# Kernel optimization log

Hardware: AMD Instinct MI355X
Metric: run time of the kernel (lower is better)

## Reference

```python
import jax, jax.numpy as jnp
import numpy as np

NUM_HEADS = 16
NUM_KV_HEADS = 4
HEAD_DIM = 64
HIDDEN = 1024
BATCH, SEQ = 2, 2048
CAUSAL = False


def _rotate_half(x):
    x1, x2 = jnp.split(x, 2, axis=-1)
    return jnp.concatenate([-x2, x1], axis=-1)


def setup_inputs() -> dict:
    key = jax.random.key(0)
    k1, k2, k3 = jax.random.split(key, 3)
    hidden_states = jax.random.normal(k1, (BATCH, SEQ, HIDDEN), dtype=jnp.float32)
    # realistic rotary tables
    inv_freq = 1.0 / (10000.0 ** (np.arange(0, HEAD_DIM, 2, dtype=np.float32) / HEAD_DIM))
    t = np.arange(SEQ, dtype=np.float32)
    freqs = np.outer(t, inv_freq)                      # [S, D/2]
    emb = np.concatenate([freqs, freqs], axis=-1)      # [S, D]
    cos = jnp.asarray(np.cos(emb), dtype=jnp.float32)
    sin = jnp.asarray(np.sin(emb), dtype=jnp.float32)
    qkv_out = (NUM_HEADS + 2 * NUM_KV_HEADS) * HEAD_DIM
    w_qkv = jax.random.normal(k2, (qkv_out, HIDDEN), dtype=jnp.float32) * (HIDDEN ** -0.5)
    w_o = jax.random.normal(k3, (HIDDEN, NUM_HEADS * HEAD_DIM), dtype=jnp.float32) * ((NUM_HEADS * HEAD_DIM) ** -0.5)
    return {"hidden_states": hidden_states, "cos": cos, "sin": sin, "w_qkv": w_qkv, "w_o": w_o}


def reference(hidden_states, cos, sin, w_qkv, w_o):
    b, s, _ = hidden_states.shape
    qkv = jnp.einsum('bsh,oh->bso', hidden_states, w_qkv)
    qkv = qkv.reshape(b, s, NUM_HEADS + 2 * NUM_KV_HEADS, HEAD_DIM)
    q = qkv[:, :, :NUM_HEADS]                                    # [b,s,Hq,d]
    k = qkv[:, :, NUM_HEADS:NUM_HEADS + NUM_KV_HEADS]            # [b,s,Hkv,d]
    v = qkv[:, :, NUM_HEADS + NUM_KV_HEADS:]                     # [b,s,Hkv,d]
    # RoPE (HF style): broadcast cos/sin [s,d] over batch and heads
    c = cos[None, :, None, :]
    sn = sin[None, :, None, :]
    q = q * c + _rotate_half(q) * sn
    k = k * c + _rotate_half(k) * sn
    # GQA: repeat kv heads to match q heads
    rep = NUM_HEADS // NUM_KV_HEADS
    k = jnp.repeat(k, rep, axis=2)
    v = jnp.repeat(v, rep, axis=2)
    scale = HEAD_DIM ** -0.5
    scores = jnp.einsum('bqhd,bkhd->bhqk', q, k) * scale
    if CAUSAL:
        mask = jnp.tril(jnp.ones((s, s), dtype=bool))
        scores = jnp.where(mask[None, None], scores, jnp.finfo(scores.dtype).min)
    probs = jax.nn.softmax(scores, axis=-1)
    attn = jnp.einsum('bhqk,bkhd->bqhd', probs, v)
    attn = attn.reshape(b, s, NUM_HEADS * HEAD_DIM)
    return jnp.einsum('bso,ho->bsh', attn, w_o)
```

## Files before the change

kernel.cpp:

```cpp
#include <hip/hip_runtime.h>
#include <hip/hip_bf16.h>

typedef unsigned short u16;
typedef unsigned int u32;
typedef __attribute__((ext_vector_type(8))) short short8;
typedef __attribute__((ext_vector_type(4))) float f32x4;
typedef __attribute__((ext_vector_type(16))) float f32x16;
typedef __attribute__((ext_vector_type(4))) u32 u32x4;

__device__ __forceinline__ u16 f2b(float f) {
    __hip_bfloat16 h = __float2bfloat16(f);
    return *reinterpret_cast<u16*>(&h);
}
__device__ __forceinline__ float b2f(u16 u) {
    __hip_bfloat16 h;
    *reinterpret_cast<u16*>(&h) = u;
    return __bfloat162float(h);
}
__device__ __forceinline__ u32 cvtpk(float lo, float hi_) {
    u32 r;
    asm("v_cvt_pk_bf16_f32 %0, %1, %2" : "=v"(r) : "v"(lo), "v"(hi_));
    return r;
}
__device__ __forceinline__ float fexp2(float x) {
    float r;
    asm("v_exp_f32 %0, %1" : "=v"(r) : "v"(x));
    return r;
}
__device__ __forceinline__ void gload16(const void* g, void* l) {
    __builtin_amdgcn_global_load_lds(
        (const __attribute__((address_space(1))) unsigned int*)g,
        (__attribute__((address_space(3))) unsigned int*)l, 16, 0, 0);
}

__global__ void convert_kernel(const float* __restrict__ X, const float* __restrict__ W1,
                               const float* __restrict__ W2,
                               u16* __restrict__ Xb, u16* __restrict__ W1b, u16* __restrict__ W2b) {
    int idx = blockIdx.x * 256 + threadIdx.x;
    const float* src; u16* dst; int off;
    if (idx < 1048576)        { src = X;  dst = Xb;  off = idx; }
    else if (idx < 1441792)   { src = W1; dst = W1b; off = idx - 1048576; }
    else                      { src = W2; dst = W2b; off = idx - 1441792; }
    float4 v = reinterpret_cast<const float4*>(src)[off];
    ushort4 o;
    o.x = f2b(v.x); o.y = f2b(v.y); o.z = f2b(v.z); o.w = f2b(v.w);
    reinterpret_cast<ushort4*>(dst)[off] = o;
}

template <typename OUT>
__global__ __launch_bounds__(256, 3) void gemm_bt(const u16* __restrict__ A, const u16* __restrict__ B,
                                                  OUT* __restrict__ C, int M, int N, int K) {
    __shared__ u16 As[2][64 * 64];
    __shared__ u16 Bs[2][128 * 64];
    const int tid = threadIdx.x;
    const int lane = tid & 63, wave = tid >> 6;
    const int wm = wave >> 1, wn = wave & 1;
    const int row16 = lane & 15, kgrp = lane >> 4;
    const int bm = blockIdx.x, bn = blockIdx.y;
    const int nk = K >> 6;

    const int r0 = tid >> 3, c0s = ((tid & 7) ^ (r0 & 7)) * 8;
    const u16* aSrc = A + (size_t)(bm * 64 + r0) * K + c0s;
    const u16* bSrc = B + (size_t)(bn * 128 + r0) * K + c0s;
    u16* const ad0 = &As[0][tid * 8];
    u16* const ad1 = &As[0][(tid + 256) * 8];
    u16* const bd0 = &Bs[0][tid * 8];
    u16* const bd1 = &Bs[0][(tid + 256) * 8];
    u16* const bd2 = &Bs[0][(tid + 512) * 8];
    u16* const bd3 = &Bs[0][(tid + 768) * 8];
    const size_t aK32 = (size_t)32 * K;

    f32x4 acc[2][4];
#pragma unroll
    for (int i = 0; i < 2; ++i)
#pragma unroll
        for (int j = 0; j < 4; ++j) acc[i][j] = {0.f, 0.f, 0.f, 0.f};

    auto stage = [&](int buf) {
        int lo = buf * 4096;
        int lob = buf * 8192;
        gload16(aSrc, ad0 + lo);
        gload16(aSrc + aK32, ad1 + lo);
        gload16(bSrc, bd0 + lob);
        gload16(bSrc + aK32, bd1 + lob);
        gload16(bSrc + 2 * aK32, bd2 + lob);
        gload16(bSrc + 3 * aK32, bd3 + lob);
        aSrc += 64; bSrc += 64;
    };

    stage(0);
    __syncthreads();
    for (int kt = 0; kt < nk; ++kt) {
        int cur = kt & 1;
        if (kt + 1 < nk) stage(cur ^ 1);
        short8 af[2][2], bfr[4][2];
#pragma unroll
        for (int mf = 0; mf < 2; ++mf) {
            int r = wm * 32 + mf * 16 + row16;
#pragma unroll
            for (int kk = 0; kk < 2; ++kk)
                af[mf][kk] = *(const short8*)&As[cur][(r * 8 + ((kk * 4 + kgrp) ^ (r & 7))) * 8];
        }
#pragma unroll
        for (int nf = 0; nf < 4; ++nf) {
            int r = wn * 64 + nf * 16 + row16;
#pragma unroll
            for (int kk = 0; kk < 2; ++kk)
                bfr[nf][kk] = *(const short8*)&Bs[cur][(r * 8 + ((kk * 4 + kgrp) ^ (r & 7))) * 8];
        }
        __builtin_amdgcn_s_setprio(1);
#pragma unroll
        for (int kk = 0; kk < 2; ++kk)
#pragma unroll
            for (int mf = 0; mf < 2; ++mf)
#pragma unroll
                for (int nf = 0; nf < 4; ++nf)
                    acc[mf][nf] = __builtin_amdgcn_mfma_f32_16x16x32_bf16(af[mf][kk], bfr[nf][kk], acc[mf][nf], 0, 0, 0);
        __builtin_amdgcn_s_setprio(0);
        __syncthreads();
    }
#pragma unroll
    for (int mf = 0; mf < 2; ++mf)
#pragma unroll
        for (int r = 0; r < 4; ++r) {
            int row = bm * 64 + wm * 32 + mf * 16 + kgrp * 4 + r;
#pragma unroll
            for (int nf = 0; nf < 4; ++nf) {
                int col = bn * 128 + wn * 64 + nf * 16 + row16;
                float v = acc[mf][nf][r];
                if constexpr (sizeof(OUT) == 2) C[(size_t)row * N + col] = f2b(v);
                else                            C[(size_t)row * N + col] = v;
            }
        }
}

__global__ void rope_kernel(const u16* __restrict__ qkv, const float* __restrict__ cosb,
                            const float* __restrict__ sinb, u16* __restrict__ Qa,
                            u16* __restrict__ Ka) {
    int idx = blockIdx.x * 256 + threadIdx.x;
    if (idx < 2097152) {
        int d = idx & 31, h = (idx >> 5) & 15, m = idx >> 9;
        int s = m & 2047, b = m >> 11;
        const u16* src = qkv + (size_t)m * 1536 + h * 64 + d;
        float q1 = b2f(src[0]), q2 = b2f(src[32]);
        float c = cosb[s * 64 + d], sn = sinb[s * 64 + d];
        u16* dst = Qa + ((size_t)(b * 16 + h) * 2048 + s) * 64 + d;
        dst[0]  = f2b((q1 * c - q2 * sn) * 0.18033688f);
        dst[32] = f2b((q2 * c + q1 * sn) * 0.18033688f);
    } else {
        int t = idx - 2097152;
        int d = t & 31, kh = (t >> 5) & 3, m = t >> 7;
        int s = m & 2047, b = m >> 11;
        const u16* src = qkv + (size_t)m * 1536 + (16 + kh) * 64 + d;
        float q1 = b2f(src[0]), q2 = b2f(src[32]);
        float c = cosb[s * 64 + d], sn = sinb[s * 64 + d];
        u16* dst = Ka + ((size_t)(b * 4 + kh) * 2048 + s) * 64 + d;
        dst[0]  = f2b(q1 * c - q2 * sn);
        dst[32] = f2b(q2 * c + q1 * sn);
    }
}

__global__ __launch_bounds__(256) void vtrans_kernel(const u16* __restrict__ qkv, u16* __restrict__ Vt) {
    __shared__ u16 T[64 * 71];
    const int tid = threadIdx.x;
    const int sblk = blockIdx.x, kh = blockIdx.y, b = blockIdx.z;
    const u16* src = qkv + (size_t)(b * 2048 + sblk * 64) * 1536 + 1280 + kh * 64;
#pragma unroll
    for (int it = 0; it < 2; ++it) {
        int u = it * 256 + tid;
        int s = u >> 3, c = u & 7;
        short8 v = *(const short8*)(src + (size_t)s * 1536 + c * 8);
#pragma unroll
        for (int i = 0; i < 8; ++i)
            T[(c * 8 + i) * 71 + s] = (u16)v[i];
    }
    __syncthreads();
    u16* dst = Vt + (size_t)(b * 4 + kh) * 64 * 2048 + sblk * 64;
#pragma unroll
    for (int it = 0; it < 2; ++it) {
        int u = it * 256 + tid;
        int d = u >> 3, s0 = (u & 7) * 8;
        short8 o;
#pragma unroll
        for (int i = 0; i < 8; ++i) o[i] = (short)T[d * 71 + s0 + i];
        *(short8*)(dst + (size_t)d * 2048 + s0) = o;
    }
}

__global__ __launch_bounds__(256, 2) void attn_kernel(const u16* __restrict__ Qa,
                                                      const u16* __restrict__ Ka,
                                                      const u16* __restrict__ Vt,
                                                      u16* __restrict__ Ob) {
    __shared__ u16 Ks[2][64 * 64];
    __shared__ u16 Vs[2][64 * 64];
    const int tid = threadIdx.x, lane = tid & 63, wave = tid >> 6;
    const int q32 = lane & 31, hi = lane >> 5;
    const int qt = blockIdx.x, h = blockIdx.y, b = blockIdx.z;
    const int kh = h >> 2;
    const u16* Qp = Qa + ((size_t)(b * 16 + h) * 2048 + qt * 128 + wave * 32) * 64;

    const int r0 = tid >> 3, c0s = ((tid & 7) ^ (r0 & 7)) * 8;
    const u16* kSrc = Ka + (size_t)(b * 4 + kh) * 2048 * 64 + (size_t)r0 * 64 + c0s;
    const u16* vSrc = Vt + (size_t)(b * 4 + kh) * 64 * 2048 + (size_t)r0 * 2048 + c0s;
    u16* const kd0 = &Ks[0][tid * 8];
    u16* const kd1 = &Ks[0][(tid + 256) * 8];
    u16* const vd0 = &Vs[0][tid * 8];
    u16* const vd1 = &Vs[0][(tid + 256) * 8];

    short8 qf[4];
#pragma unroll
    for (int dt = 0; dt < 4; ++dt)
        qf[dt] = *(const short8*)(Qp + q32 * 64 + dt * 16 + hi * 8);

    f32x16 oacc[2];
#pragma unroll
    for (int i = 0; i < 2; ++i)
#pragma unroll
        for (int r = 0; r < 16; ++r) oacc[i][r] = 0.f;
    float lpx = 0.f, lpy = 0.f;

    auto stageKV = [&](int buf) {
        int lo = buf * 4096;
        gload16(kSrc,           kd0 + lo);
        gload16(kSrc + 32 * 64, kd1 + lo);
        gload16(vSrc,             vd0 + lo);
        gload16(vSrc + 32 * 2048, vd1 + lo);
        kSrc += 4096; vSrc += 64;
    };

    stageKV(0);
    __syncthreads();
    for (int kvt = 0; kvt < 32; ++kvt) {
        const int cur = kvt & 1;
        if (kvt + 1 < 32) stageKV(cur ^ 1);

        f32x16 S[2];
#pragma unroll
        for (int j = 0; j < 2; ++j)
#pragma unroll
            for (int r = 0; r < 16; ++r) S[j][r] = 0.f;
        __builtin_amdgcn_s_setprio(1);
#pragma unroll
        for (int kt2 = 0; kt2 < 2; ++kt2) {
            int krow = kt2 * 32 + q32;
#pragma unroll
            for (int dt = 0; dt < 4; ++dt) {
                short8 kf = *(const short8*)&Ks[cur][(krow * 8 + ((dt * 2 + hi) ^ (krow & 7))) * 8];
                S[kt2] = __builtin_amdgcn_mfma_f32_32x32x16_bf16(kf, qf[dt], S[kt2], 0, 0, 0);
            }
        }
        __builtin_amdgcn_s_setprio(0);

#pragma unroll
        for (int kt2 = 0; kt2 < 2; ++kt2)
#pragma unroll
            for (int r = 0; r < 16; r += 2) {
                float p0 = fexp2(S[kt2][r]);
                float p1 = fexp2(S[kt2][r + 1]);
                S[kt2][r] = p0; S[kt2][r + 1] = p1;
                lpx += p0; lpy += p1;
            }

        __builtin_amdgcn_s_setprio(1);
#pragma unroll
        for (int kc = 0; kc < 4; ++kc) {
            const int kt2 = kc >> 1, R = (kc & 1) * 8;
            u32 a0 = cvtpk(S[kt2][R + 0], S[kt2][R + 1]);
            u32 b0 = cvtpk(S[kt2][R + 4], S[kt2][R + 5]);
            asm("v_permlane32_swap_b32 %0, %1" : "+v"(a0), "+v"(b0));
            u32 a1 = cvtpk(S[kt2][R + 2], S[kt2][R + 3]);
            u32 b1 = cvtpk(S[kt2][R + 6], S[kt2][R + 7]);
            asm("v_permlane32_swap_b32 %0, %1" : "+v"(a1), "+v"(b1));
            u32x4 pw; pw[0] = a0; pw[1] = a1; pw[2] = b0; pw[3] = b1;
            short8 pf = __builtin_bit_cast(short8, pw);
#pragma unroll
            for (int dt2 = 0; dt2 < 2; ++dt2) {
                int vrow = dt2 * 32 + q32;
                short8 vf = *(const short8*)&Vs[cur][(vrow * 8 + ((kc * 2 + hi) ^ (vrow & 7))) * 8];
                oacc[dt2] = __builtin_amdgcn_mfma_f32_32x32x16_bf16(vf, pf, oacc[dt2], 0, 0, 0);
            }
        }
        __builtin_amdgcn_s_setprio(0);
        __syncthreads();
    }

    float lpart = lpx + lpy;
    float l = lpart + __shfl_xor(lpart, 32);
    float inv = 1.f / l;
    const size_t mbase = ((size_t)(b * 2048 + qt * 128 + wave * 32 + q32)) * 1024 + h * 64;
#pragma unroll
    for (int dt2 = 0; dt2 < 2; ++dt2)
#pragma unroll
        for (int rq = 0; rq < 4; ++rq) {
            ushort4 o;
            o.x = f2b(oacc[dt2][rq * 4 + 0] * inv);
            o.y = f2b(oacc[dt2][rq * 4 + 1] * inv);
            o.z = f2b(oacc[dt2][rq * 4 + 2] * inv);
            o.w = f2b(oacc[dt2][rq * 4 + 3] * inv);
            *(ushort4*)&Ob[mbase + dt2 * 32 + rq * 8 + hi * 4] = o;
        }
}

extern "C" void kernel_launch(void* const* d_in, const int* in_sizes, int n_in,
                              void* d_out, int out_size, void* d_ws, size_t ws_size,
                              hipStream_t stream) {
    const float* X    = (const float*)d_in[0];
    const float* cosb = (const float*)d_in[1];
    const float* sinb = (const float*)d_in[2];
    const float* Wqkv = (const float*)d_in[3];
    const float* Wo   = (const float*)d_in[4];
    float* out = (float*)d_out;
    char* ws = (char*)d_ws;

    u16* Xbf    = (u16*)(ws);
    u16* Wqkvbf = (u16*)(ws + 8388608);
    u16* Wobf   = (u16*)(ws + 11534336);
    u16* QKV    = (u16*)(ws + 13631488);
    u16* Qa     = (u16*)(ws + 26214400);
    u16* Ka     = (u16*)(ws + 34603008);
    u16* Vt     = (u16*)(ws + 36700160);
    u16* attnb  = Xbf;

    convert_kernel<<<6656, 256, 0, stream>>>(X, Wqkv, Wo, Xbf, Wqkvbf, Wobf);
    gemm_bt<u16><<<dim3(64, 12), 256, 0, stream>>>(Xbf, Wqkvbf, QKV, 4096, 1536, 1024);
    rope_kernel<<<10240, 256, 0, stream>>>(QKV, cosb, sinb, Qa, Ka);
    vtrans_kernel<<<dim3(32, 4, 2), 256, 0, stream>>>(QKV, Vt);
    attn_kernel<<<dim3(16, 16, 2), 256, 0, stream>>>(Qa, Ka, Vt, attnb);
    gemm_bt<float><<<dim3(64, 8), 256, 0, stream>>>(attnb, Wobf, out, 4096, 1024, 1024);
}
```

Baseline: 166.6 us.

## Fuse RoPE into QKV GEMM epilogue and register-stage KV loads in attention

Adds a specialized QKV GEMM whose epilogue applies RoPE and scaling and writes Q and K directly in head-major layout, while V goes to a compact temporary buffer. This removes the separate rope kernel and the full QKV intermediate round trip. The attention kernel also changes from direct global-to-LDS loads to register-staged loads that are prefetched two tiles ahead, with a transposed swizzled LDS layout and an explicit waitcnt/barrier. The risks are higher register pressure and scattered 2-byte epilogue stores.

```diff
diff --git a/kernel.cpp b/kernel.cpp
--- a/kernel.cpp
+++ b/kernel.cpp
@@ -47,6 +47,266 @@
     reinterpret_cast<ushort4*>(dst)[off] = o;
 }
 
+__global__ __launch_bounds__(256, 3) void gemm_qkv(const u16* __restrict__ A, const u16* __restrict__ B,
+                                                   const float* __restrict__ cosb, const float* __restrict__ sinb,
+                                                   u16* __restrict__ Qa, u16* __restrict__ Ka,
+                                                   u16* __restrict__ Vtmp) {
+    __shared__ u16 As[2][64 * 64];
+    __shared__ u16 Bs[2][128 * 64];
+    const int tid = threadIdx.x;
+    const int lane = tid & 63, wave = tid >> 6;
+    const int wm = wave >> 1, wn = wave & 1;
+    const int row16 = lane & 15, kgrp = lane >> 4;
+    const int bm = blockIdx.x, bn = blockIdx.y;
+    const int K = 1024;
+
+    const int r0 = tid >> 3, c0s = ((tid & 7) ^ (r0 & 7)) * 8;
+    const u16* aSrc = A + (size_t)(bm * 64 + r0) * K + c0s;
+    const u16* bSrc = B + (size_t)(bn * 128 + r0) * K + c0s;
+    u16* const ad0 = &As[0][tid * 8];
+    u16* const ad1 = &As[0][(tid + 256) * 8];
+    u16* const bd0 = &Bs[0][tid * 8];
+    u16* const bd1 = &Bs[0][(tid + 256) * 8];
+    u16* const bd2 = &Bs[0][(tid + 512) * 8];
+    u16* const bd3 = &Bs[0][(tid + 768) * 8];
+    const size_t aK32 = (size_t)32 * K;
+
+    f32x4 acc[2][4];
+#pragma unroll
+    for (int i = 0; i < 2; ++i)
+#pragma unroll
+        for (int j = 0; j < 4; ++j) acc[i][j] = {0.f, 0.f, 0.f, 0.f};
+
+    auto stage = [&](int buf) {
+        int lo = buf * 4096;
+        int lob = buf * 8192;
+        gload16(aSrc, ad0 + lo);
+        gload16(aSrc + aK32, ad1 + lo);
+        gload16(bSrc, bd0 + lob);
+        gload16(bSrc + aK32, bd1 + lob);
+        gload16(bSrc + 2 * aK32, bd2 + lob);
+        gload16(bSrc + 3 * aK32, bd3 + lob);
+        aSrc += 64; bSrc += 64;
+    };
+
+    stage(0);
+    __syncthreads();
+    for (int kt = 0; kt < 16; ++kt) {
+        int cur = kt & 1;
+        if (kt + 1 < 16) stage(cur ^ 1);
+        short8 af[2][2], bfr[4][2];
+#pragma unroll
+        for (int mf = 0; mf < 2; ++mf) {
+            int r = wm * 32 + mf * 16 + row16;
+#pragma unroll
+            for (int kk = 0; kk < 2; ++kk)
+                af[mf][kk] = *(const short8*)&As[cur][(r * 8 + ((kk * 4 + kgrp) ^ (r & 7))) * 8];
+        }
+#pragma unroll
+        for (int nf = 0; nf < 4; ++nf) {
+            int r = wn * 64 + nf * 16 + row16;
+#pragma unroll
+            for (int kk = 0; kk < 2; ++kk)
+                bfr[nf][kk] = *(const short8*)&Bs[cur][(r * 8 + ((kk * 4 + kgrp) ^ (r & 7))) * 8];
+        }
+        __builtin_amdgcn_s_setprio(1);
+#pragma unroll
+        for (int kk = 0; kk < 2; ++kk)
+#pragma unroll
+            for (int mf = 0; mf < 2; ++mf)
+#pragma unroll
+                for (int nf = 0; nf < 4; ++nf)
+                    acc[mf][nf] = __builtin_amdgcn_mfma_f32_16x16x32_bf16(af[mf][kk], bfr[nf][kk], acc[mf][nf], 0, 0, 0);
+        __builtin_amdgcn_s_setprio(0);
+        __syncthreads();
+    }
+
+#pragma unroll
+    for (int mf = 0; mf < 2; ++mf)
+#pragma unroll
+        for (int r = 0; r < 4; ++r) {
+            int m = bm * 64 + wm * 32 + mf * 16 + kgrp * 4 + r;
+            int s = m & 2047, bb = m >> 11;
+            float v0 = acc[mf][0][r], v1 = acc[mf][1][r], v2 = acc[mf][2][r], v3 = acc[mf][3][r];
+            if (bn < 10) {
+                float c0 = cosb[s * 64 + row16],       c1 = cosb[s * 64 + 16 + row16];
+                float n0 = sinb[s * 64 + row16],       n1 = sinb[s * 64 + 16 + row16];
+                float o0 = v0 * c0 - v2 * n0, o1 = v1 * c1 - v3 * n1;
+                float o2 = v2 * c0 + v0 * n0, o3 = v3 * c1 + v1 * n1;
+                u16* dst;
+                if (bn < 8) {
+                    int h = bn * 2 + wn;
+                    dst = Qa + ((size_t)(bb * 16 + h) * 2048 + s) * 64;
+                    o0 *= 0.18033688f; o1 *= 0.18033688f; o2 *= 0.18033688f; o3 *= 0.18033688f;
+                } else {
+                    int kh = (bn - 8) * 2 + wn;
+                    dst = Ka + ((size_t)(bb * 4 + kh) * 2048 + s) * 64;
+                }
+                dst[row16]      = f2b(o0);
+                dst[row16 + 16] = f2b(o1);
+                dst[row16 + 32] = f2b(o2);
+                dst[row16 + 48] = f2b(o3);
+            } else {
+                u16* dst = Vtmp + (size_t)m * 256 + (bn - 10) * 128 + wn * 64;
+                dst[row16]      = f2b(v0);
+                dst[row16 + 16] = f2b(v1);
+                dst[row16 + 32] = f2b(v2);
+                dst[row16 + 48] = f2b(v3);
+            }
+        }
+}
+
+__global__ __launch_bounds__(256) void vtrans_kernel(const u16* __restrict__ Vtmp, u16* __restrict__ Vt) {
+    __shared__ u16 T[64 * 71];
+    const int tid = threadIdx.x;
+    const int sblk = blockIdx.x, kh = blockIdx.y, b = blockIdx.z;
+    const u16* src = Vtmp + (size_t)(b * 2048 + sblk * 64) * 256 + kh * 64;
+#pragma unroll
+    for (int it = 0; it < 2; ++it) {
+        int u = it * 256 + tid;
+        int s = u >> 3, c = u & 7;
+        short8 v = *(const short8*)(src + (size_t)s * 256 + c * 8);
+#pragma unroll
+        for (int i = 0; i < 8; ++i)
+            T[(c * 8 + i) * 71 + s] = (u16)v[i];
+    }
+    __syncthreads();
+    u16* dst = Vt + (size_t)(b * 4 + kh) * 64 * 2048 + sblk * 64;
+#pragma unroll
+    for (int it = 0; it < 2; ++it) {
+        int u = it * 256 + tid;
+        int d = u >> 3, s0 = (u & 7) * 8;
+        short8 o;
+#pragma unroll
+        for (int i = 0; i < 8; ++i) o[i] = (short)T[d * 71 + s0 + i];
+        *(short8*)(dst + (size_t)d * 2048 + s0) = o;
+    }
+}
+
+__global__ __launch_bounds__(256, 2) void attn_kernel(const u16* __restrict__ Qa,
+                                                      const u16* __restrict__ Ka,
+                                                      const u16* __restrict__ Vt,
+                                                      u16* __restrict__ Ob) {
+    __shared__ u16 Ks[2][4096];
+    __shared__ u16 Vs[2][4096];
+    const int tid = threadIdx.x, lane = tid & 63, wave = tid >> 6;
+    const int q32 = lane & 31, hi = lane >> 5;
+    const int qt = blockIdx.x, h = blockIdx.y, b = blockIdx.z;
+    const int kh = h >> 2;
+    const u16* Qp = Qa + ((size_t)(b * 16 + h) * 2048 + qt * 128 + wave * 32) * 64;
+
+    const int lrow = tid >> 3, lc = tid & 7;
+    const u16* kSrc = Ka + (size_t)(b * 4 + kh) * 2048 * 64 + (size_t)lrow * 64 + lc * 8;
+    const u16* vSrc = Vt + (size_t)(b * 4 + kh) * 64 * 2048 + (size_t)lrow * 2048 + lc * 8;
+    const int wk = (lc * 64 + (lrow ^ lc)) * 8;
+
+    int rb[8];
+#pragma unroll
+    for (int c = 0; c < 8; ++c) rb[c] = (c * 64 + (q32 ^ c)) * 8;
+
+    short8 qf[4];
+#pragma unroll
+    for (int dt = 0; dt < 4; ++dt)
+        qf[dt] = *(const short8*)(Qp + q32 * 64 + dt * 16 + hi * 8);
+
+    f32x16 oacc[2];
+#pragma unroll
+    for (int i = 0; i < 2; ++i)
+#pragma unroll
+        for (int r = 0; r < 16; ++r) oacc[i][r] = 0.f;
+    float lpx = 0.f, lpy = 0.f;
+
+    short8 kr0, kr1, vr0, vr1;
+    auto LOAD = [&]() {
+        kr0 = *(const short8*)kSrc;
+        kr1 = *(const short8*)(kSrc + 2048);
+        vr0 = *(const short8*)vSrc;
+        vr1 = *(const short8*)(vSrc + 65536);
+        kSrc += 4096; vSrc += 64;
+    };
+    auto WRITE = [&](int buf) {
+        *(short8*)&Ks[buf][wk]       = kr0;
+        *(short8*)&Ks[buf][wk + 256] = kr1;
+        *(short8*)&Vs[buf][wk]       = vr0;
+        *(short8*)&Vs[buf][wk + 256] = vr1;
+    };
+
+    LOAD();
+    WRITE(0);
+    LOAD();
+    asm volatile("s_waitcnt lgkmcnt(0)\n\ts_barrier" ::: "memory");
+
+    for (int kvt = 0; kvt < 32; ++kvt) {
+        const int cur = kvt & 1;
+        if (kvt + 1 < 32) WRITE(cur ^ 1);
+        if (kvt + 2 < 32) LOAD();
+
+        f32x16 S[2];
+#pragma unroll
+        for (int j = 0; j < 2; ++j)
+#pragma unroll
+            for (int r = 0; r < 16; ++r) S[j][r] = 0.f;
+        __builtin_amdgcn_s_setprio(1);
+#pragma unroll
+        for (int kt2 = 0; kt2 < 2; ++kt2) {
+#pragma unroll
+            for (int dt = 0; dt < 4; ++dt) {
+                short8 kf = *(const short8*)&Ks[cur][rb[dt * 2 + hi] + kt2 * 256];
+                S[kt2] = __builtin_amdgcn_mfma_f32_32x32x16_bf16(kf, qf[dt], S[kt2], 0, 0, 0);
+            }
+        }
+        __builtin_amdgcn_s_setprio(0);
+
+#pragma unroll
+        for (int kt2 = 0; kt2 < 2; ++kt2)
+#pragma unroll
+            for (int r = 0; r < 16; r += 2) {
+                float p0 = fexp2(S[kt2][r]);
+                float p1 = fexp2(S[kt2][r + 1]);
+                S[kt2][r] = p0; S[kt2][r + 1] = p1;
+                lpx += p0; lpy += p1;
+            }
+
+        __builtin_amdgcn_s_setprio(1);
+#pragma unroll
+        for (int kc = 0; kc < 4; ++kc) {
+            const int kt2 = kc >> 1, R = (kc & 1) * 8;
+            u32 a0 = cvtpk(S[kt2][R + 0], S[kt2][R + 1]);
+            u32 b0 = cvtpk(S[kt2][R + 4], S[kt2][R + 5]);
+            asm("v_permlane32_swap_b32 %0, %1" : "+v"(a0), "+v"(b0));
+            u32 a1 = cvtpk(S[kt2][R + 2], S[kt2][R + 3]);
+            u32 b1 = cvtpk(S[kt2][R + 6], S[kt2][R + 7]);
+            asm("v_permlane32_swap_b32 %0, %1" : "+v"(a1), "+v"(b1));
+            u32x4 pw; pw[0] = a0; pw[1] = a1; pw[2] = b0; pw[3] = b1;
+            short8 pf = __builtin_bit_cast(short8, pw);
+#pragma unroll
+            for (int dt2 = 0; dt2 < 2; ++dt2) {
+                short8 vf = *(const short8*)&Vs[cur][rb[kc * 2 + hi] + dt2 * 256];
+                oacc[dt2] = __builtin_amdgcn_mfma_f32_32x32x16_bf16(vf, pf, oacc[dt2], 0, 0, 0);
+            }
+        }
+        __builtin_amdgcn_s_setprio(0);
+
+        asm volatile("s_waitcnt lgkmcnt(0)\n\ts_barrier" ::: "memory");
+    }
+
+    float lpart = lpx + lpy;
+    float l = lpart + __shfl_xor(lpart, 32);
+    float inv = 1.f / l;
+    const size_t mbase = ((size_t)(b * 2048 + qt * 128 + wave * 32 + q32)) * 1024 + h * 64;
+#pragma unroll
+    for (int dt2 = 0; dt2 < 2; ++dt2)
+#pragma unroll
+        for (int rq = 0; rq < 4; ++rq) {
+            ushort4 o;
+            o.x = f2b(oacc[dt2][rq * 4 + 0] * inv);
+            o.y = f2b(oacc[dt2][rq * 4 + 1] * inv);
+            o.z = f2b(oacc[dt2][rq * 4 + 2] * inv);
+            o.w = f2b(oacc[dt2][rq * 4 + 3] * inv);
+            *(ushort4*)&Ob[mbase + dt2 * 32 + rq * 8 + hi * 4] = o;
+        }
+}
+
 template <typename OUT>
 __global__ __launch_bounds__(256, 3) void gemm_bt(const u16* __restrict__ A, const u16* __restrict__ B,
                                                   OUT* __restrict__ C, int M, int N, int K) {
@@ -134,173 +394,6 @@
         }
 }
 
-__global__ void rope_kernel(const u16* __restrict__ qkv, const float* __restrict__ cosb,
-                            const float* __restrict__ sinb, u16* __restrict__ Qa,
-                            u16* __restrict__ Ka) {
-    int idx = blockIdx.x * 256 + threadIdx.x;
-    if (idx < 2097152) {
-        int d = idx & 31, h = (idx >> 5) & 15, m = idx >> 9;
-        int s = m & 2047, b = m >> 11;
-        const u16* src = qkv + (size_t)m * 1536 + h * 64 + d;
-        float q1 = b2f(src[0]), q2 = b2f(src[32]);
-        float c = cosb[s * 64 + d], sn = sinb[s * 64 + d];
-        u16* dst = Qa + ((size_t)(b * 16 + h) * 2048 + s) * 64 + d;
-        dst[0]  = f2b((q1 * c - q2 * sn) * 0.18033688f);
-        dst[32] = f2b((q2 * c + q1 * sn) * 0.18033688f);
-    } else {
-        int t = idx - 2097152;
-        int d = t & 31, kh = (t >> 5) & 3, m = t >> 7;
-        int s = m & 2047, b = m >> 11;
-        const u16* src = qkv + (size_t)m * 1536 + (16 + kh) * 64 + d;
-        float q1 = b2f(src[0]), q2 = b2f(src[32]);
-        float c = cosb[s * 64 + d], sn = sinb[s * 64 + d];
-        u16* dst = Ka + ((size_t)(b * 4 + kh) * 2048 + s) * 64 + d;
-        dst[0]  = f2b(q1 * c - q2 * sn);
-        dst[32] = f2b(q2 * c + q1 * sn);
-    }
-}
-
-__global__ __launch_bounds__(256) void vtrans_kernel(const u16* __restrict__ qkv, u16* __restrict__ Vt) {
-    __shared__ u16 T[64 * 71];
-    const int tid = threadIdx.x;
-    const int sblk = blockIdx.x, kh = blockIdx.y, b = blockIdx.z;
-    const u16* src = qkv + (size_t)(b * 2048 + sblk * 64) * 1536 + 1280 + kh * 64;
-#pragma unroll
-    for (int it = 0; it < 2; ++it) {
-        int u = it * 256 + tid;
-        int s = u >> 3, c = u & 7;
-        short8 v = *(const short8*)(src + (size_t)s * 1536 + c * 8);
-#pragma unroll
-        for (int i = 0; i < 8; ++i)
-            T[(c * 8 + i) * 71 + s] = (u16)v[i];
-    }
-    __syncthreads();
-    u16* dst = Vt + (size_t)(b * 4 + kh) * 64 * 2048 + sblk * 64;
-#pragma unroll
-    for (int it = 0; it < 2; ++it) {
-        int u = it * 256 + tid;
-        int d = u >> 3, s0 = (u & 7) * 8;
-        short8 o;
-#pragma unroll
-        for (int i = 0; i < 8; ++i) o[i] = (short)T[d * 71 + s0 + i];
-        *(short8*)(dst + (size_t)d * 2048 + s0) = o;
-    }
-}
-
-__global__ __launch_bounds__(256, 2) void attn_kernel(const u16* __restrict__ Qa,
-                                                      const u16* __restrict__ Ka,
-                                                      const u16* __restrict__ Vt,
-                                                      u16* __restrict__ Ob) {
-    __shared__ u16 Ks[2][64 * 64];
-    __shared__ u16 Vs[2][64 * 64];
-    const int tid = threadIdx.x, lane = tid & 63, wave = tid >> 6;
-    const int q32 = lane & 31, hi = lane >> 5;
-    const int qt = blockIdx.x, h = blockIdx.y, b = blockIdx.z;
-    const int kh = h >> 2;
-    const u16* Qp = Qa + ((size_t)(b * 16 + h) * 2048 + qt * 128 + wave * 32) * 64;
-
-    const int r0 = tid >> 3, c0s = ((tid & 7) ^ (r0 & 7)) * 8;
-    const u16* kSrc = Ka + (size_t)(b * 4 + kh) * 2048 * 64 + (size_t)r0 * 64 + c0s;
-    const u16* vSrc = Vt + (size_t)(b * 4 + kh) * 64 * 2048 + (size_t)r0 * 2048 + c0s;
-    u16* const kd0 = &Ks[0][tid * 8];
-    u16* const kd1 = &Ks[0][(tid + 256) * 8];
-    u16* const vd0 = &Vs[0][tid * 8];
-    u16* const vd1 = &Vs[0][(tid + 256) * 8];
-
-    short8 qf[4];
-#pragma unroll
-    for (int dt = 0; dt < 4; ++dt)
-        qf[dt] = *(const short8*)(Qp + q32 * 64 + dt * 16 + hi * 8);
-
-    f32x16 oacc[2];
-#pragma unroll
-    for (int i = 0; i < 2; ++i)
-#pragma unroll
-        for (int r = 0; r < 16; ++r) oacc[i][r] = 0.f;
-    float lpx = 0.f, lpy = 0.f;
-
-    auto stageKV = [&](int buf) {
-        int lo = buf * 4096;
-        gload16(kSrc,           kd0 + lo);
-        gload16(kSrc + 32 * 64, kd1 + lo);
-        gload16(vSrc,             vd0 + lo);
-        gload16(vSrc + 32 * 2048, vd1 + lo);
-        kSrc += 4096; vSrc += 64;
-    };
-
-    stageKV(0);
-    __syncthreads();
-    for (int kvt = 0; kvt < 32; ++kvt) {
-        const int cur = kvt & 1;
-        if (kvt + 1 < 32) stageKV(cur ^ 1);
-
-        f32x16 S[2];
-#pragma unroll
-        for (int j = 0; j < 2; ++j)
-#pragma unroll
-            for (int r = 0; r < 16; ++r) S[j][r] = 0.f;
-        __builtin_amdgcn_s_setprio(1);
-#pragma unroll
-        for (int kt2 = 0; kt2 < 2; ++kt2) {
-            int krow = kt2 * 32 + q32;
-#pragma unroll
-            for (int dt = 0; dt < 4; ++dt) {
-                short8 kf = *(const short8*)&Ks[cur][(krow * 8 + ((dt * 2 + hi) ^ (krow & 7))) * 8];
-                S[kt2] = __builtin_amdgcn_mfma_f32_32x32x16_bf16(kf, qf[dt], S[kt2], 0, 0, 0);
-            }
-        }
-        __builtin_amdgcn_s_setprio(0);
-
-#pragma unroll
-        for (int kt2 = 0; kt2 < 2; ++kt2)
-#pragma unroll
-            for (int r = 0; r < 16; r += 2) {
-                float p0 = fexp2(S[kt2][r]);
-                float p1 = fexp2(S[kt2][r + 1]);
-                S[kt2][r] = p0; S[kt2][r + 1] = p1;
-                lpx += p0; lpy += p1;
-            }
-
-        __builtin_amdgcn_s_setprio(1);
-#pragma unroll
-        for (int kc = 0; kc < 4; ++kc) {
-            const int kt2 = kc >> 1, R = (kc & 1) * 8;
-            u32 a0 = cvtpk(S[kt2][R + 0], S[kt2][R + 1]);
-            u32 b0 = cvtpk(S[kt2][R + 4], S[kt2][R + 5]);
-            asm("v_permlane32_swap_b32 %0, %1" : "+v"(a0), "+v"(b0));
-            u32 a1 = cvtpk(S[kt2][R + 2], S[kt2][R + 3]);
-            u32 b1 = cvtpk(S[kt2][R + 6], S[kt2][R + 7]);
-            asm("v_permlane32_swap_b32 %0, %1" : "+v"(a1), "+v"(b1));
-            u32x4 pw; pw[0] = a0; pw[1] = a1; pw[2] = b0; pw[3] = b1;
-            short8 pf = __builtin_bit_cast(short8, pw);
-#pragma unroll
-            for (int dt2 = 0; dt2 < 2; ++dt2) {
-                int vrow = dt2 * 32 + q32;
-                short8 vf = *(const short8*)&Vs[cur][(vrow * 8 + ((kc * 2 + hi) ^ (vrow & 7))) * 8];
-                oacc[dt2] = __builtin_amdgcn_mfma_f32_32x32x16_bf16(vf, pf, oacc[dt2], 0, 0, 0);
-            }
-        }
-        __builtin_amdgcn_s_setprio(0);
-        __syncthreads();
-    }
-
-    float lpart = lpx + lpy;
-    float l = lpart + __shfl_xor(lpart, 32);
-    float inv = 1.f / l;
-    const size_t mbase = ((size_t)(b * 2048 + qt * 128 + wave * 32 + q32)) * 1024 + h * 64;
-#pragma unroll
-    for (int dt2 = 0; dt2 < 2; ++dt2)
-#pragma unroll
-        for (int rq = 0; rq < 4; ++rq) {
-            ushort4 o;
-            o.x = f2b(oacc[dt2][rq * 4 + 0] * inv);
-            o.y = f2b(oacc[dt2][rq * 4 + 1] * inv);
-            o.z = f2b(oacc[dt2][rq * 4 + 2] * inv);
-            o.w = f2b(oacc[dt2][rq * 4 + 3] * inv);
-            *(ushort4*)&Ob[mbase + dt2 * 32 + rq * 8 + hi * 4] = o;
-        }
-}
-
 extern "C" void kernel_launch(void* const* d_in, const int* in_sizes, int n_in,
                               void* d_out, int out_size, void* d_ws, size_t ws_size,
                               hipStream_t stream) {
@@ -315,16 +408,15 @@
     u16* Xbf    = (u16*)(ws);
     u16* Wqkvbf = (u16*)(ws + 8388608);
     u16* Wobf   = (u16*)(ws + 11534336);
-    u16* QKV    = (u16*)(ws + 13631488);
+    u16* Vtmp   = (u16*)(ws + 13631488);
     u16* Qa     = (u16*)(ws + 26214400);
     u16* Ka     = (u16*)(ws + 34603008);
     u16* Vt     = (u16*)(ws + 36700160);
     u16* attnb  = Xbf;
 
     convert_kernel<<<6656, 256, 0, stream>>>(X, Wqkv, Wo, Xbf, Wqkvbf, Wobf);
-    gemm_bt<u16><<<dim3(64, 12), 256, 0, stream>>>(Xbf, Wqkvbf, QKV, 4096, 1536, 1024);
-    rope_kernel<<<10240, 256, 0, stream>>>(QKV, cosb, sinb, Qa, Ka);
-    vtrans_kernel<<<dim3(32, 4, 2), 256, 0, stream>>>(QKV, Vt);
+    gemm_qkv<<<dim3(64, 12), 256, 0, stream>>>(Xbf, Wqkvbf, cosb, sinb, Qa, Ka, Vtmp);
+    vtrans_kernel<<<dim3(32, 4, 2), 256, 0, stream>>>(Vtmp, Vt);
     attn_kernel<<<dim3(16, 16, 2), 256, 0, stream>>>(Qa, Ka, Vt, attnb);
     gemm_bt<float><<<dim3(64, 8), 256, 0, stream>>>(attnb, Wobf, out, 4096, 1024, 1024);
 }
```

Result: faster. 157.0 us (-5.8%).
